# Kernel optimization log

Measured on AMD Instinct MI355X. Metric: run time of the kernel, lower is better.

## Reference

```python
import jax, jax.numpy as jnp
import numpy as np

N_HEADS = 8
N_HIDDEN = 32  # out_features // n_heads
NEG_SLOPE = 0.21
MASK_VAL = -1000000.0  # precision == '32'


def setup_inputs() -> dict:
    key = jax.random.key(0)
    k1, k2, k3, k4, k5 = jax.random.split(key, 5)
    B, N, Fin = 4, 512, 256
    HF = N_HEADS * N_HIDDEN
    h = jax.random.normal(k1, (B, N, Fin), dtype=jnp.float32)
    adj_mat = jax.random.randint(k2, (1, N, N, 1), 0, 2, dtype=jnp.int32)
    W_l = jax.random.normal(k3, (Fin, HF), dtype=jnp.float32) * 0.05
    W_r = jax.random.normal(k4, (Fin, HF), dtype=jnp.float32) * 0.05
    attn_w = jax.random.normal(k5, (N_HIDDEN,), dtype=jnp.float32) * 0.05
    return {"h": h, "adj_mat": adj_mat, "W_l": W_l, "W_r": W_r, "attn_w": attn_w}


def reference(h, adj_mat, W_l, W_r, attn_w):
    B, N, _ = h.shape
    H, F = N_HEADS, N_HIDDEN
    g_l = (h @ W_l).reshape(B, N, H, F)
    g_r = (h @ W_r).reshape(B, N, H, F)
    # torch repeat/repeat_interleave semantics: g_sum[b,i,j] = g_l[b,j] + g_r[b,i]
    g_sum = g_l[:, None, :, :, :] + g_r[:, :, None, :, :]  # (B, i, j, H, F)
    act = jnp.where(g_sum >= 0, g_sum, NEG_SLOPE * g_sum)
    e = jnp.einsum('bijhf,f->bijh', act, attn_w)  # (B, N, N, H)
    e = jnp.where(adj_mat == 0, MASK_VAL, e)
    a = jax.nn.softmax(e, axis=2)
    # dropout is identity in eval mode
    attn_res = jnp.einsum('bijh,bjhf->bihf', a, g_r)
    return attn_res.reshape(B, N, H * F)  # is_concat=True
```

## Files before the change

### kernel.cpp

```cpp
#include <hip/hip_runtime.h>
#include <math.h>

#define BB 4
#define NN 512
#define FIN 256
#define NH 8
#define FD 32
#define HF 256
#define MASKH (-60000.0f)
#define CA 0.605f
#define CB 0.395f
#define IT 32
#define ESTR 268
#define GTS 260

typedef _Float16 h2_t __attribute__((ext_vector_type(2)));
union H2U { unsigned u; h2_t h; };
typedef __fp16 v8h __attribute__((ext_vector_type(8)));
typedef float v4f __attribute__((ext_vector_type(4)));
union U8 { uint4 u4; v8h h; };

__device__ __forceinline__ h2_t pkrtz(float a, float b) {
  auto r = __builtin_amdgcn_cvt_pkrtz(a, b);
  union { decltype(r) f; h2_t h; } u;
  u.f = r;
  return u.h;
}
__device__ __forceinline__ unsigned pkrtz_u(float a, float b) {
  H2U u; u.h = pkrtz(a, b);
  return u.u;
}

__device__ __forceinline__ float acc2(unsigned g, h2_t q, h2_t u, float acc) {
  H2U v; v.u = g;
  h2_t s = v.h + q;
  H2U a; a.h = s; a.u &= 0x7fff7fffu;
  return __builtin_amdgcn_fdot2(a.h, u, acc, false);
}

__device__ __forceinline__ float score16(uint4 g0, uint4 g1, uint4 g2, uint4 g3,
                                         const h2_t* qh, const h2_t* uh,
                                         float init) {
  float e0 = init, e1 = 0.f;
  e0 = acc2(g0.x, qh[0], uh[0], e0);
  e1 = acc2(g0.y, qh[1], uh[1], e1);
  e0 = acc2(g0.z, qh[2], uh[2], e0);
  e1 = acc2(g0.w, qh[3], uh[3], e1);
  e0 = acc2(g1.x, qh[4], uh[4], e0);
  e1 = acc2(g1.y, qh[5], uh[5], e1);
  e0 = acc2(g1.z, qh[6], uh[6], e0);
  e1 = acc2(g1.w, qh[7], uh[7], e1);
  e0 = acc2(g2.x, qh[8], uh[8], e0);
  e1 = acc2(g2.y, qh[9], uh[9], e1);
  e0 = acc2(g2.z, qh[10], uh[10], e0);
  e1 = acc2(g2.w, qh[11], uh[11], e1);
  e0 = acc2(g3.x, qh[12], uh[12], e0);
  e1 = acc2(g3.y, qh[13], uh[13], e1);
  e0 = acc2(g3.z, qh[14], uh[14], e0);
  e1 = acc2(g3.w, qh[15], uh[15], e1);
  return e0 + e1;
}

__global__ __launch_bounds__(256) void gemm_dual(
    const float* __restrict__ h, const float* __restrict__ Wl,
    const float* __restrict__ Wr, _Float16* __restrict__ glh,
    float* __restrict__ gr) {
  const int t = threadIdx.x;
  const int row0 = blockIdx.x * 8;
  const float* __restrict__ W = blockIdx.y ? Wr : Wl;

  float acc[8] = {0.f, 0.f, 0.f, 0.f, 0.f, 0.f, 0.f, 0.f};
  const float* Wp = W + t;
  const float* hp = h + (size_t)row0 * FIN;

#pragma unroll 2
  for (int k4 = 0; k4 < FIN / 4; ++k4) {
    float4 hv[8];
#pragma unroll
    for (int r = 0; r < 8; ++r)
      hv[r] = *(const float4*)(hp + r * FIN + 4 * k4);
#pragma unroll
    for (int kk = 0; kk < 4; ++kk) {
      const float w = Wp[(size_t)(4 * k4 + kk) * HF];
#pragma unroll
      for (int r = 0; r < 8; ++r) {
        const float hval = (kk == 0) ? hv[r].x
                         : (kk == 1) ? hv[r].y
                         : (kk == 2) ? hv[r].z : hv[r].w;
        acc[r] = fmaf(hval, w, acc[r]);
      }
    }
  }

  if (blockIdx.y == 0) {
    _Float16* gp = glh + (size_t)row0 * HF + t;
#pragma unroll
    for (int r = 0; r < 8; ++r) gp[(size_t)r * HF] = (_Float16)acc[r];
  } else {
    float* gp = gr + (size_t)row0 * HF + t;
#pragma unroll
    for (int r = 0; r < 8; ++r) gp[(size_t)r * HF] = acc[r];
  }
}

__global__ __launch_bounds__(256, 2) void gat_attn(
    const _Float16* __restrict__ glh, const float* __restrict__ gr,
    const int* __restrict__ adj, const float* __restrict__ aw,
    float* __restrict__ out) {
  __shared__ __align__(16) unsigned ubuf[32 * GTS];
  __shared__ __align__(16) unsigned e_s[IT][ESTR];
  __shared__ float Al_s[NN];
  __shared__ float inv_l[IT];

  const int t = threadIdx.x;
  const int hh = blockIdx.x;
  const int i0 = blockIdx.y * IT;
  const int b = blockIdx.z;
  const int ii = t & 31;
  const int jg = t >> 5;

  uint4* gl4 = (uint4*)ubuf;

  const _Float16* glp = glh + (size_t)b * NN * HF + hh * FD;

  h2_t wv[16], uh[16], qh[16];
  float a_r = 0.f;
  {
    const float* qp = gr + (size_t)(b * NN + i0 + ii) * HF + hh * FD;
#pragma unroll
    for (int f4 = 0; f4 < 8; ++f4) {
      const float4 w4 = *(const float4*)(aw + 4 * f4);
      const float4 q4 = *(const float4*)(qp + 4 * f4);
      wv[2 * f4] = pkrtz(CA * w4.x, CA * w4.y);
      wv[2 * f4 + 1] = pkrtz(CA * w4.z, CA * w4.w);
      uh[2 * f4] = pkrtz(CB * w4.x, CB * w4.y);
      uh[2 * f4 + 1] = pkrtz(CB * w4.z, CB * w4.w);
      qh[2 * f4] = pkrtz(q4.x, q4.y);
      qh[2 * f4 + 1] = pkrtz(q4.z, q4.w);
      a_r = fmaf(CA * w4.x, q4.x, a_r);
      a_r = fmaf(CA * w4.y, q4.y, a_r);
      a_r = fmaf(CA * w4.z, q4.z, a_r);
      a_r = fmaf(CA * w4.w, q4.w, a_r);
    }
  }

#pragma unroll
  for (int c = 0; c < 2; ++c) {
    const int j = t + 256 * c;
    const uint4* gp = (const uint4*)(glp + (size_t)j * HF);
    const uint4 g0 = gp[0], g1 = gp[1], g2 = gp[2], g3 = gp[3];
    gl4[0 * NN + j] = g0;
    gl4[1 * NN + j] = g1;
    gl4[2 * NN + j] = g2;
    gl4[3 * NN + j] = g3;
    float s0 = 0.f, s1 = 0.f;
    H2U v;
#define ALD(gu, i)                                                  \
  v.u = gu.x; s0 = __builtin_amdgcn_fdot2(v.h, wv[i+0], s0, false); \
  v.u = gu.y; s1 = __builtin_amdgcn_fdot2(v.h, wv[i+1], s1, false); \
  v.u = gu.z; s0 = __builtin_amdgcn_fdot2(v.h, wv[i+2], s0, false); \
  v.u = gu.w; s1 = __builtin_amdgcn_fdot2(v.h, wv[i+3], s1, false);
    ALD(g0, 0) ALD(g1, 4) ALD(g2, 8) ALD(g3, 12)
#undef ALD
    Al_s[j] = s0 + s1;
  }
  __syncthreads();

  {
    unsigned* erow = &e_s[ii][jg * 32];
    const int* adjp = adj + (size_t)(i0 + ii) * NN + jg * 64;
#pragma unroll 4
    for (int g4 = 0; g4 < 16; ++g4) {
      const int4 a4 = ((const int4*)adjp)[g4];
      const int j = jg * 64 + 4 * g4;
      float e0 = score16(gl4[0 * NN + j], gl4[1 * NN + j], gl4[2 * NN + j],
                         gl4[3 * NN + j], qh, uh, Al_s[j] + a_r);
      float e1 = score16(gl4[0 * NN + j + 1], gl4[1 * NN + j + 1],
                         gl4[2 * NN + j + 1], gl4[3 * NN + j + 1], qh, uh,
                         Al_s[j + 1] + a_r);
      float e2 = score16(gl4[0 * NN + j + 2], gl4[1 * NN + j + 2],
                         gl4[2 * NN + j + 2], gl4[3 * NN + j + 2], qh, uh,
                         Al_s[j + 2] + a_r);
      float e3 = score16(gl4[0 * NN + j + 3], gl4[1 * NN + j + 3],
                         gl4[2 * NN + j + 3], gl4[3 * NN + j + 3], qh, uh,
                         Al_s[j + 3] + a_r);
      e0 = a4.x ? e0 : MASKH;
      e1 = a4.y ? e1 : MASKH;
      e2 = a4.z ? e2 : MASKH;
      e3 = a4.w ? e3 : MASKH;
      erow[2 * g4] = pkrtz_u(e0, e1);
      erow[2 * g4 + 1] = pkrtz_u(e2, e3);
    }
  }
  __syncthreads();

  {
    const int fq = t & 7;
    const int jp0 = t >> 3;
    const float* gbase = gr + (size_t)b * NN * HF + hh * FD + fq * 4;
#pragma unroll
    for (int s2 = 0; s2 < 8; ++s2) {
      const int jp = jp0 + 32 * s2;
      const float4 r0 = *(const float4*)(gbase + (size_t)(2 * jp) * HF);
      const float4 r1 = *(const float4*)(gbase + (size_t)(2 * jp + 1) * HF);
      ubuf[(4 * fq + 0) * GTS + jp] = pkrtz_u(r0.x, r1.x);
      ubuf[(4 * fq + 1) * GTS + jp] = pkrtz_u(r0.y, r1.y);
      ubuf[(4 * fq + 2) * GTS + jp] = pkrtz_u(r0.z, r1.z);
      ubuf[(4 * fq + 3) * GTS + jp] = pkrtz_u(r0.w, r1.w);
    }
    const int row = t >> 3;
    const int l8 = t & 7;
    unsigned* erow = &e_s[row][0];
    float m = MASKH;
#pragma unroll
    for (int c = 0; c < 32; ++c) {
      H2U v; v.u = erow[l8 + 8 * c];
      m = fmaxf(m, fmaxf((float)v.h.x, (float)v.h.y));
    }
#pragma unroll
    for (int off = 1; off < 8; off <<= 1) m = fmaxf(m, __shfl_xor(m, off));
    float s = 0.f;
#pragma unroll
    for (int c = 0; c < 32; ++c) {
      H2U v; v.u = erow[l8 + 8 * c];
      const float p0 = __expf((float)v.h.x - m);
      const float p1 = __expf((float)v.h.y - m);
      s += p0 + p1;
      erow[l8 + 8 * c] = pkrtz_u(p0, p1);
    }
#pragma unroll
    for (int off = 1; off < 8; off <<= 1) s += __shfl_xor(s, off);
    if (l8 == 0) inv_l[row] = 1.f / s;
  }
  __syncthreads();

  {
    const int lane = t & 63;
    const int wv3 = t >> 6;
    const int Mt = wv3 & 1, Nt = wv3 >> 1;
    const int l16 = lane & 15, q = lane >> 4;
    const unsigned* arow = &e_s[Mt * 16 + l16][0];
    const unsigned* brow = &ubuf[(Nt * 16 + l16) * GTS];
    v4f acc = {0.f, 0.f, 0.f, 0.f};
#pragma unroll
    for (int s = 0; s < 16; ++s) {
      U8 a; a.u4 = *(const uint4*)(arow + 16 * s + 4 * q);
      U8 bf; bf.u4 = *(const uint4*)(brow + 16 * s + 4 * q);
      acc = __builtin_amdgcn_mfma_f32_16x16x32_f16(a.h, bf.h, acc, 0, 0, 0);
    }
    float* op = out + (size_t)(b * NN + i0 + Mt * 16 + q * 4) * HF + hh * FD +
                Nt * 16 + l16;
#pragma unroll
    for (int r = 0; r < 4; ++r) {
      op[(size_t)r * HF] = acc[r] * inv_l[Mt * 16 + q * 4 + r];
    }
  }
}

extern "C" void kernel_launch(void* const* d_in, const int* in_sizes, int n_in,
                              void* d_out, int out_size, void* d_ws,
                              size_t ws_size, hipStream_t stream) {
  const float* h = (const float*)d_in[0];
  const int* adj = (const int*)d_in[1];
  const float* Wl = (const float*)d_in[2];
  const float* Wr = (const float*)d_in[3];
  const float* aw = (const float*)d_in[4];
  float* out = (float*)d_out;

  _Float16* glh = (_Float16*)d_ws;
  float* gr = (float*)((char*)d_ws + (size_t)BB * NN * HF * 2);

  dim3 gg(BB * NN / 8, 2, 1);
  gemm_dual<<<gg, 256, 0, stream>>>(h, Wl, Wr, glh, gr);

  dim3 ga(NH, NN / IT, BB);
  gat_attn<<<ga, 256, 0, stream>>>(glh, gr, adj, aw, out);
}
```

Baseline: 105.1 us.

## Halve row tile, store g_r in fp16, swizzle LDS, split-K MFMA

The attention row tile shrinks from 32 to 16 rows, doubling the grid and raising the occupancy hint to 3 blocks per SM. To keep all four waves busy, the MFMA stage splits K across wave pairs and reduces the partial sums through shared memory. g_r is now written in fp16 by the projection GEMM, which halves its traffic and lets the V-transpose use byte-permute packing instead of float conversion. The gl and Al shared arrays get XOR and padding swizzles to reduce bank conflicts, and the adjacency loads are hoisted to the start of the kernel. The cost is that g_l is restaged once per 16 rows instead of per 32, and the query vector now carries extra fp16 rounding.

```diff
diff --git a/kernel.cpp b/kernel.cpp
--- a/kernel.cpp
+++ b/kernel.cpp
@@ -10,9 +10,11 @@
 #define MASKH (-60000.0f)
 #define CA 0.605f
 #define CB 0.395f
-#define IT 32
+#define IT 16
 #define ESTR 268
 #define GTS 260
+#define GLX(j) ((j) ^ (((j) >> 5) & 7))
+#define ALX(j) ((j) + ((j) >> 5))
 
 typedef _Float16 h2_t __attribute__((ext_vector_type(2)));
 union H2U { unsigned u; h2_t h; };
@@ -64,7 +66,7 @@
 __global__ __launch_bounds__(256) void gemm_dual(
     const float* __restrict__ h, const float* __restrict__ Wl,
     const float* __restrict__ Wr, _Float16* __restrict__ glh,
-    float* __restrict__ gr) {
+    _Float16* __restrict__ grh) {
   const int t = threadIdx.x;
   const int row0 = blockIdx.x * 8;
   const float* __restrict__ W = blockIdx.y ? Wr : Wl;
@@ -92,56 +94,67 @@
     }
   }
 
-  if (blockIdx.y == 0) {
-    _Float16* gp = glh + (size_t)row0 * HF + t;
-#pragma unroll
-    for (int r = 0; r < 8; ++r) gp[(size_t)r * HF] = (_Float16)acc[r];
-  } else {
-    float* gp = gr + (size_t)row0 * HF + t;
-#pragma unroll
-    for (int r = 0; r < 8; ++r) gp[(size_t)r * HF] = acc[r];
-  }
-}
-
-__global__ __launch_bounds__(256, 2) void gat_attn(
-    const _Float16* __restrict__ glh, const float* __restrict__ gr,
+  _Float16* gp = (blockIdx.y ? grh : glh) + (size_t)row0 * HF + t;
+#pragma unroll
+  for (int r = 0; r < 8; ++r) gp[(size_t)r * HF] = (_Float16)acc[r];
+}
+
+__global__ __launch_bounds__(256, 3) void gat_attn(
+    const _Float16* __restrict__ glh, const _Float16* __restrict__ grh,
     const int* __restrict__ adj, const float* __restrict__ aw,
     float* __restrict__ out) {
-  __shared__ __align__(16) unsigned ubuf[32 * GTS];
+  __shared__ __align__(16) unsigned ubuf[8320];
   __shared__ __align__(16) unsigned e_s[IT][ESTR];
-  __shared__ float Al_s[NN];
+  __shared__ float Al_s[544];
   __shared__ float inv_l[IT];
 
   const int t = threadIdx.x;
   const int hh = blockIdx.x;
   const int i0 = blockIdx.y * IT;
   const int b = blockIdx.z;
-  const int ii = t & 31;
-  const int jg = t >> 5;
+  const int ii = t & 15;
+  const int jg = t >> 4;
 
   uint4* gl4 = (uint4*)ubuf;
 
   const _Float16* glp = glh + (size_t)b * NN * HF + hh * FD;
+
+  const int* adjp = adj + (size_t)(i0 + ii) * NN + jg * 32;
+  const int4 a0 = ((const int4*)adjp)[0];
+  const int4 a1 = ((const int4*)adjp)[1];
+  const int4 a2 = ((const int4*)adjp)[2];
+  const int4 a3 = ((const int4*)adjp)[3];
+  const int4 a4 = ((const int4*)adjp)[4];
+  const int4 a5 = ((const int4*)adjp)[5];
+  const int4 a6 = ((const int4*)adjp)[6];
+  const int4 a7 = ((const int4*)adjp)[7];
 
   h2_t wv[16], uh[16], qh[16];
   float a_r = 0.f;
   {
-    const float* qp = gr + (size_t)(b * NN + i0 + ii) * HF + hh * FD;
 #pragma unroll
     for (int f4 = 0; f4 < 8; ++f4) {
       const float4 w4 = *(const float4*)(aw + 4 * f4);
-      const float4 q4 = *(const float4*)(qp + 4 * f4);
       wv[2 * f4] = pkrtz(CA * w4.x, CA * w4.y);
       wv[2 * f4 + 1] = pkrtz(CA * w4.z, CA * w4.w);
       uh[2 * f4] = pkrtz(CB * w4.x, CB * w4.y);
       uh[2 * f4 + 1] = pkrtz(CB * w4.z, CB * w4.w);
-      qh[2 * f4] = pkrtz(q4.x, q4.y);
-      qh[2 * f4 + 1] = pkrtz(q4.z, q4.w);
-      a_r = fmaf(CA * w4.x, q4.x, a_r);
-      a_r = fmaf(CA * w4.y, q4.y, a_r);
-      a_r = fmaf(CA * w4.z, q4.z, a_r);
-      a_r = fmaf(CA * w4.w, q4.w, a_r);
-    }
+    }
+    const uint4* qp4 =
+        (const uint4*)(grh + (size_t)(b * NN + i0 + ii) * HF + hh * FD);
+    const uint4 q0 = qp4[0], q1 = qp4[1], q2 = qp4[2], q3 = qp4[3];
+    H2U z;
+    z.u = q0.x; qh[0] = z.h;  z.u = q0.y; qh[1] = z.h;
+    z.u = q0.z; qh[2] = z.h;  z.u = q0.w; qh[3] = z.h;
+    z.u = q1.x; qh[4] = z.h;  z.u = q1.y; qh[5] = z.h;
+    z.u = q1.z; qh[6] = z.h;  z.u = q1.w; qh[7] = z.h;
+    z.u = q2.x; qh[8] = z.h;  z.u = q2.y; qh[9] = z.h;
+    z.u = q2.z; qh[10] = z.h; z.u = q2.w; qh[11] = z.h;
+    z.u = q3.x; qh[12] = z.h; z.u = q3.y; qh[13] = z.h;
+    z.u = q3.z; qh[14] = z.h; z.u = q3.w; qh[15] = z.h;
+#pragma unroll
+    for (int f2 = 0; f2 < 16; ++f2)
+      a_r = __builtin_amdgcn_fdot2(qh[f2], wv[f2], a_r, false);
   }
 
 #pragma unroll
@@ -149,10 +162,11 @@
     const int j = t + 256 * c;
     const uint4* gp = (const uint4*)(glp + (size_t)j * HF);
     const uint4 g0 = gp[0], g1 = gp[1], g2 = gp[2], g3 = gp[3];
-    gl4[0 * NN + j] = g0;
-    gl4[1 * NN + j] = g1;
-    gl4[2 * NN + j] = g2;
-    gl4[3 * NN + j] = g3;
+    const int jx = GLX(j);
+    gl4[0 * NN + jx] = g0;
+    gl4[1 * NN + jx] = g1;
+    gl4[2 * NN + jx] = g2;
+    gl4[3 * NN + jx] = g3;
     float s0 = 0.f, s1 = 0.f;
     H2U v;
 #define ALD(gu, i)                                                  \
@@ -162,97 +176,104 @@
   v.u = gu.w; s1 = __builtin_amdgcn_fdot2(v.h, wv[i+3], s1, false);
     ALD(g0, 0) ALD(g1, 4) ALD(g2, 8) ALD(g3, 12)
 #undef ALD
-    Al_s[j] = s0 + s1;
+    Al_s[ALX(j)] = s0 + s1;
   }
   __syncthreads();
 
   {
-    unsigned* erow = &e_s[ii][jg * 32];
-    const int* adjp = adj + (size_t)(i0 + ii) * NN + jg * 64;
-#pragma unroll 4
-    for (int g4 = 0; g4 < 16; ++g4) {
-      const int4 a4 = ((const int4*)adjp)[g4];
-      const int j = jg * 64 + 4 * g4;
-      float e0 = score16(gl4[0 * NN + j], gl4[1 * NN + j], gl4[2 * NN + j],
-                         gl4[3 * NN + j], qh, uh, Al_s[j] + a_r);
-      float e1 = score16(gl4[0 * NN + j + 1], gl4[1 * NN + j + 1],
-                         gl4[2 * NN + j + 1], gl4[3 * NN + j + 1], qh, uh,
-                         Al_s[j + 1] + a_r);
-      float e2 = score16(gl4[0 * NN + j + 2], gl4[1 * NN + j + 2],
-                         gl4[2 * NN + j + 2], gl4[3 * NN + j + 2], qh, uh,
-                         Al_s[j + 2] + a_r);
-      float e3 = score16(gl4[0 * NN + j + 3], gl4[1 * NN + j + 3],
-                         gl4[2 * NN + j + 3], gl4[3 * NN + j + 3], qh, uh,
-                         Al_s[j + 3] + a_r);
-      e0 = a4.x ? e0 : MASKH;
-      e1 = a4.y ? e1 : MASKH;
-      e2 = a4.z ? e2 : MASKH;
-      e3 = a4.w ? e3 : MASKH;
-      erow[2 * g4] = pkrtz_u(e0, e1);
-      erow[2 * g4 + 1] = pkrtz_u(e2, e3);
-    }
+    unsigned* erow = &e_s[ii][jg * 16];
+    const int j0 = jg * 32;
+#define SJ(j)                                                       \
+  score16(gl4[0 * NN + GLX(j)], gl4[1 * NN + GLX(j)],               \
+          gl4[2 * NN + GLX(j)], gl4[3 * NN + GLX(j)], qh, uh,       \
+          Al_s[ALX(j)] + a_r)
+#define DO_G4(g4, A)                                                \
+  {                                                                 \
+    const int j = j0 + 4 * (g4);                                    \
+    float e0 = SJ(j), e1 = SJ(j + 1), e2 = SJ(j + 2), e3 = SJ(j + 3); \
+    e0 = (A).x ? e0 : MASKH;                                        \
+    e1 = (A).y ? e1 : MASKH;                                        \
+    e2 = (A).z ? e2 : MASKH;                                        \
+    e3 = (A).w ? e3 : MASKH;                                        \
+    erow[2 * (g4)] = pkrtz_u(e0, e1);                               \
+    erow[2 * (g4) + 1] = pkrtz_u(e2, e3);                           \
+  }
+    DO_G4(0, a0) DO_G4(1, a1) DO_G4(2, a2) DO_G4(3, a3)
+    DO_G4(4, a4) DO_G4(5, a5) DO_G4(6, a6) DO_G4(7, a7)
+#undef SJ
+#undef DO_G4
   }
   __syncthreads();
 
   {
     const int fq = t & 7;
     const int jp0 = t >> 3;
-    const float* gbase = gr + (size_t)b * NN * HF + hh * FD + fq * 4;
+    const unsigned* gbase =
+        (const unsigned*)(grh + (size_t)b * NN * HF + hh * FD) + 2 * fq;
 #pragma unroll
     for (int s2 = 0; s2 < 8; ++s2) {
       const int jp = jp0 + 32 * s2;
-      const float4 r0 = *(const float4*)(gbase + (size_t)(2 * jp) * HF);
-      const float4 r1 = *(const float4*)(gbase + (size_t)(2 * jp + 1) * HF);
-      ubuf[(4 * fq + 0) * GTS + jp] = pkrtz_u(r0.x, r1.x);
-      ubuf[(4 * fq + 1) * GTS + jp] = pkrtz_u(r0.y, r1.y);
-      ubuf[(4 * fq + 2) * GTS + jp] = pkrtz_u(r0.z, r1.z);
-      ubuf[(4 * fq + 3) * GTS + jp] = pkrtz_u(r0.w, r1.w);
-    }
-    const int row = t >> 3;
-    const int l8 = t & 7;
+      const uint2 A = *(const uint2*)(gbase + (size_t)(2 * jp) * 128);
+      const uint2 Bv = *(const uint2*)(gbase + (size_t)(2 * jp + 1) * 128);
+      ubuf[(4 * fq + 0) * GTS + jp] = __builtin_amdgcn_perm(Bv.x, A.x, 0x05040100u);
+      ubuf[(4 * fq + 1) * GTS + jp] = __builtin_amdgcn_perm(Bv.x, A.x, 0x07060302u);
+      ubuf[(4 * fq + 2) * GTS + jp] = __builtin_amdgcn_perm(Bv.y, A.y, 0x05040100u);
+      ubuf[(4 * fq + 3) * GTS + jp] = __builtin_amdgcn_perm(Bv.y, A.y, 0x07060302u);
+    }
+    const int row = t >> 4;
+    const int l16 = t & 15;
     unsigned* erow = &e_s[row][0];
     float m = MASKH;
 #pragma unroll
-    for (int c = 0; c < 32; ++c) {
-      H2U v; v.u = erow[l8 + 8 * c];
+    for (int c = 0; c < 16; ++c) {
+      H2U v; v.u = erow[l16 + 16 * c];
       m = fmaxf(m, fmaxf((float)v.h.x, (float)v.h.y));
     }
 #pragma unroll
-    for (int off = 1; off < 8; off <<= 1) m = fmaxf(m, __shfl_xor(m, off));
+    for (int off = 1; off < 16; off <<= 1) m = fmaxf(m, __shfl_xor(m, off));
     float s = 0.f;
 #pragma unroll
-    for (int c = 0; c < 32; ++c) {
-      H2U v; v.u = erow[l8 + 8 * c];
+    for (int c = 0; c < 16; ++c) {
+      H2U v; v.u = erow[l16 + 16 * c];
       const float p0 = __expf((float)v.h.x - m);
       const float p1 = __expf((float)v.h.y - m);
       s += p0 + p1;
-      erow[l8 + 8 * c] = pkrtz_u(p0, p1);
-    }
-#pragma unroll
-    for (int off = 1; off < 8; off <<= 1) s += __shfl_xor(s, off);
-    if (l8 == 0) inv_l[row] = 1.f / s;
+      erow[l16 + 16 * c] = pkrtz_u(p0, p1);
+    }
+#pragma unroll
+    for (int off = 1; off < 16; off <<= 1) s += __shfl_xor(s, off);
+    if (l16 == 0) inv_l[row] = 1.f / s;
   }
   __syncthreads();
 
   {
     const int lane = t & 63;
     const int wv3 = t >> 6;
-    const int Mt = wv3 & 1, Nt = wv3 >> 1;
+    const int Nt = wv3 & 1, Kh = wv3 >> 1;
     const int l16 = lane & 15, q = lane >> 4;
-    const unsigned* arow = &e_s[Mt * 16 + l16][0];
+    const unsigned* arow = &e_s[l16][0];
     const unsigned* brow = &ubuf[(Nt * 16 + l16) * GTS];
     v4f acc = {0.f, 0.f, 0.f, 0.f};
 #pragma unroll
-    for (int s = 0; s < 16; ++s) {
+    for (int s = 8 * Kh; s < 8 * Kh + 8; ++s) {
       U8 a; a.u4 = *(const uint4*)(arow + 16 * s + 4 * q);
       U8 bf; bf.u4 = *(const uint4*)(brow + 16 * s + 4 * q);
       acc = __builtin_amdgcn_mfma_f32_16x16x32_f16(a.h, bf.h, acc, 0, 0, 0);
     }
-    float* op = out + (size_t)(b * NN + i0 + Mt * 16 + q * 4) * HF + hh * FD +
-                Nt * 16 + l16;
-#pragma unroll
-    for (int r = 0; r < 4; ++r) {
-      op[(size_t)r * HF] = acc[r] * inv_l[Mt * 16 + q * 4 + r];
+    if (Kh) {
+#pragma unroll
+      for (int r = 0; r < 4; ++r)
+        Al_s[Nt * 256 + (q * 4 + r) * 16 + l16] = acc[r];
+    }
+    __syncthreads();
+    if (!Kh) {
+      float* op = out + (size_t)(b * NN + i0 + q * 4) * HF + hh * FD +
+                  Nt * 16 + l16;
+#pragma unroll
+      for (int r = 0; r < 4; ++r)
+        op[(size_t)r * HF] =
+            (acc[r] + Al_s[Nt * 256 + (q * 4 + r) * 16 + l16]) *
+            inv_l[q * 4 + r];
     }
   }
 }
@@ -268,11 +289,11 @@
   float* out = (float*)d_out;
 
   _Float16* glh = (_Float16*)d_ws;
-  float* gr = (float*)((char*)d_ws + (size_t)BB * NN * HF * 2);
+  _Float16* grh = (_Float16*)((char*)d_ws + (size_t)BB * NN * HF * 2);
 
   dim3 gg(BB * NN / 8, 2, 1);
-  gemm_dual<<<gg, 256, 0, stream>>>(h, Wl, Wr, glh, gr);
+  gemm_dual<<<gg, 256, 0, stream>>>(h, Wl, Wr, glh, grh);
 
   dim3 ga(NH, NN / IT, BB);
-  gat_attn<<<ga, 256, 0, stream>>>(glh, gr, adj, aw, out);
-}
+  gat_attn<<<ga, 256, 0, stream>>>(glh, grh, adj, aw, out);
+}
```

Result: no change. 106.8 us (+1.5%).
